# Optimization experiments

Hardware: AMD Instinct MI355X
Metric: run time of the kernel (lower is better)

## Reference

```python
import jax, jax.numpy as jnp
import numpy as np

D_MODEL = 256
HIDDEN = 64
R = 1            # corr_radius
MAX_DELTA = 4.0  # max_delta_px
GROUPS = 8       # _gn_groups(64)
B, H, W = 2, 128, 128


def grid_sample_border(img, grid):
    """Bilinear grid_sample, padding_mode='border', align_corners=False.
    img: [B,C,H,W], grid: [B,Hg,Wg,2] (x,y in [-1,1]-ish). -> [B,C,Hg,Wg]"""
    Bi, C, Hi, Wi = img.shape
    x = (grid[..., 0] + 1.0) * (Wi * 0.5) - 0.5
    y = (grid[..., 1] + 1.0) * (Hi * 0.5) - 0.5
    x = jnp.clip(x, 0.0, Wi - 1.0)
    y = jnp.clip(y, 0.0, Hi - 1.0)
    x0 = jnp.floor(x); y0 = jnp.floor(y)
    wx = (x - x0)[:, None]; wy = (y - y0)[:, None]
    x0i = x0.astype(jnp.int32); y0i = y0.astype(jnp.int32)
    x1i = jnp.minimum(x0i + 1, Wi - 1); y1i = jnp.minimum(y0i + 1, Hi - 1)
    imgf = img.reshape(Bi, C, Hi * Wi)
    def gat(im, yi, xi):  # im [C,HW], yi/xi [Hg,Wg]
        return im[:, (yi * Wi + xi).reshape(-1)].reshape(C, *yi.shape)
    g = jax.vmap(gat)
    v00 = g(imgf, y0i, x0i); v01 = g(imgf, y0i, x1i)
    v10 = g(imgf, y1i, x0i); v11 = g(imgf, y1i, x1i)
    return (v00 * (1 - wx) * (1 - wy) + v01 * wx * (1 - wy)
            + v10 * (1 - wx) * wy + v11 * wx * wy)


def l2norm(x, axis):
    n = jnp.sqrt(jnp.sum(x * x, axis=axis, keepdims=True))
    return x / jnp.maximum(n, 1e-12)


def conv2d(x, w, pad):
    return jax.lax.conv_general_dilated(x, w, (1, 1), [(pad, pad), (pad, pad)],
                                        dimension_numbers=('NCHW', 'OIHW', 'NCHW'))


def group_norm(x, gamma, beta, groups=GROUPS, eps=1e-5):
    Bi, C, Hi, Wi = x.shape
    xg = x.reshape(Bi, groups, C // groups, Hi, Wi)
    mu = xg.mean(axis=(2, 3, 4), keepdims=True)
    var = xg.var(axis=(2, 3, 4), keepdims=True)
    xn = ((xg - mu) * jax.lax.rsqrt(var + eps)).reshape(Bi, C, Hi, Wi)
    return xn * gamma[None, :, None, None] + beta[None, :, None, None]


def conv_gn_gelu(x, w, g, b, pad):
    return jax.nn.gelu(group_norm(conv2d(x, w, pad), g, b), approximate=False)


def make_grid(h, w):
    xs = (jnp.arange(w, dtype=jnp.float32) + 0.5) * (2.0 / w) - 1.0
    ys = (jnp.arange(h, dtype=jnp.float32) + 0.5) * (2.0 / h) - 1.0
    gx, gy = jnp.meshgrid(xs, ys, indexing='xy')
    return jnp.stack([gx, gy], axis=-1)[None]  # [1,H,W,2]


def setup_inputs() -> dict:
    key = jax.random.key(0)
    ks = jax.random.split(key, 12)
    in_ch = D_MODEL * 3 + 2 + 1 + (2 * R + 1) ** 2  # 780
    def w(k, o, i, kh, kw):
        return (jax.random.normal(k, (o, i, kh, kw), jnp.float32)
                / np.sqrt(i * kh * kw).astype(np.float32))
    return {
        'feat_A_map': jax.random.normal(ks[0], (B, D_MODEL, H, W), jnp.float32),
        'feat_B_map': jax.random.normal(ks[1], (B, D_MODEL, H, W), jnp.float32),
        'coarse_warp': jax.random.uniform(ks[2], (B, H, W, 2), jnp.float32, -1.0, 1.0),
        'confidence': jax.random.uniform(ks[3], (B, H, W), jnp.float32),
        'enc1_w': w(ks[4], HIDDEN, in_ch, 1, 1),
        'gn1_g': jnp.ones(HIDDEN, jnp.float32), 'gn1_b': jnp.zeros(HIDDEN, jnp.float32),
        'enc2_w': w(ks[5], HIDDEN, HIDDEN, 3, 3),
        'gn2_g': jnp.ones(HIDDEN, jnp.float32), 'gn2_b': jnp.zeros(HIDDEN, jnp.float32),
        'enc3_w': w(ks[6], HIDDEN, HIDDEN, 3, 3),
        'gn3_g': jnp.ones(HIDDEN, jnp.float32), 'gn3_b': jnp.zeros(HIDDEN, jnp.float32),
        'delta_w': w(ks[7], 2, HIDDEN, 3, 3) * 0.01, 'delta_b': jnp.zeros(2, jnp.float32),
        'conf_w': w(ks[8], 1, HIDDEN, 3, 3) * 0.01, 'conf_b': jnp.zeros(1, jnp.float32),
    }


def reference(feat_A_map, feat_B_map, coarse_warp, confidence,
              enc1_w, gn1_g, gn1_b, enc2_w, gn2_g, gn2_b, enc3_w, gn3_g, gn3_b,
              delta_w, delta_b, conf_w, conf_b):
    cw = jnp.clip(jnp.nan_to_num(coarse_warp, nan=0.0, posinf=1.5, neginf=-1.5), -1.5, 1.5)
    route = jax.lax.stop_gradient(cw)  # detached routing warp
    warped_B = grid_sample_border(feat_B_map, route)
    src = make_grid(H, W)
    disp = jnp.transpose(cw - src, (0, 3, 1, 2))  # [B,2,H,W]
    conf = jnp.clip(jnp.nan_to_num(confidence, nan=0.0, posinf=1.0, neginf=0.0), 0.0, 1.0)
    conf_chw = conf[:, None]
    # warp-aware correlation over (2R+1)^2 offsets, vectorized via vmap
    fa_n = l2norm(jnp.nan_to_num(feat_A_map, nan=0.0, posinf=0.0, neginf=0.0), axis=1)
    fb = jnp.nan_to_num(feat_B_map, nan=0.0, posinf=0.0, neginf=0.0)
    offs = jnp.asarray([[2.0 * dx / W, 2.0 * dy / H]
                        for dy in range(-R, R + 1) for dx in range(-R, R + 1)],
                       dtype=jnp.float32)  # [K,2]
    grids = jnp.clip(jnp.nan_to_num(route[None] + offs[:, None, None, None, :],
                                    nan=0.0, posinf=1.5, neginf=-1.5), -1.5, 1.5)
    sampled = jax.vmap(grid_sample_border, in_axes=(None, 0))(fb, grids)  # [K,B,C,H,W]
    corr = jnp.transpose(jnp.sum(fa_n[None] * l2norm(sampled, axis=2), axis=2),
                         (1, 0, 2, 3))  # [B,K,H,W]
    x = jnp.concatenate([feat_A_map, warped_B, jnp.abs(feat_A_map - warped_B),
                         disp, conf_chw, corr], axis=1)
    h = conv_gn_gelu(x, enc1_w, gn1_g, gn1_b, 0)
    h = conv_gn_gelu(h, enc2_w, gn2_g, gn2_b, 1)
    h = conv_gn_gelu(h, enc3_w, gn3_g, gn3_b, 1)
    delta_raw = jnp.transpose(jnp.tanh(conv2d(h, delta_w, 1)
                                       + delta_b[None, :, None, None]), (0, 2, 3, 1))
    scale = jnp.asarray([2.0 * MAX_DELTA / W, 2.0 * MAX_DELTA / H], jnp.float32)
    fine_warp = jnp.clip(jnp.nan_to_num(route + delta_raw * scale,
                                        nan=0.0, posinf=1.5, neginf=-1.5), -1.5, 1.5)
    conf_delta = (conv2d(h, conf_w, 1) + conf_b[None, :, None, None])[:, 0]
    p = jnp.clip(conf, 1e-4, 1.0 - 1e-4)
    base_logit = jnp.log(p) - jnp.log1p(-p)
    refined_logits = base_logit + 0.5 * conf_delta
    refined_conf = jnp.clip(jax.nn.sigmoid(refined_logits), 0.0, 1.0)
    return (fine_warp, refined_conf, refined_logits)
```

## Files before the change

### kernel.cpp

```cpp
#include <hip/hip_runtime.h>
#include <hip/hip_bf16.h>
#include <math.h>

#define B_ 2
#define H_ 128
#define W_ 128
#define C_ 256
#define HID 64
#define PIX_PER (H_*W_)
#define NPIX (B_*PIX_PER)
#define K1STEPS 25
#define K3STEPS 18
#define SROW 264

using f32x4 = __attribute__((ext_vector_type(4))) float;
using s16x8 = __attribute__((ext_vector_type(8))) short;
using u16x2 = __attribute__((ext_vector_type(2))) unsigned short;
using u16x4 = __attribute__((ext_vector_type(4))) unsigned short;
using u16x8 = __attribute__((ext_vector_type(8))) unsigned short;

__device__ __forceinline__ float bf2f(unsigned short u) {
    return __uint_as_float(((unsigned)u) << 16);
}
__device__ __forceinline__ unsigned short f2bf(float f) {
    unsigned u = __float_as_uint(f);
    u += 0x7FFFu + ((u >> 16) & 1u);
    return (unsigned short)(u >> 16);
}
__device__ __forceinline__ float clean15(float v) {
    if (v != v) v = 0.f;
    return fminf(fmaxf(v, -1.5f), 1.5f);
}
__device__ __forceinline__ float clean01(float v) {
    if (v != v) v = 0.f;
    return fminf(fmaxf(v, 0.f), 1.f);
}

__global__ __launch_bounds__(256) void k_transpose(const float* __restrict__ A,
                                                   const float* __restrict__ Bm,
                                                   unsigned short* __restrict__ faT,
                                                   unsigned short* __restrict__ fbT,
                                                   const float* __restrict__ w1,
                                                   const float* __restrict__ w2,
                                                   const float* __restrict__ w3,
                                                   unsigned short* __restrict__ p1,
                                                   unsigned short* __restrict__ p2,
                                                   unsigned short* __restrict__ p3)
{
    if (blockIdx.z == 4) {
        if (blockIdx.y != 0 || blockIdx.x >= 61) return;
        int t = blockIdx.x * 256 + threadIdx.x;
        if (t < 6400) {
            int lane = t & 63, nt = (t >> 6) & 3, ks = t >> 8;
            int n = nt * 16 + (lane & 15);
            int kb = ks * 32 + 8 * (lane >> 4);
#pragma unroll
            for (int j = 0; j < 8; j++) {
                int k = kb + j;
                p1[(size_t)t * 8 + j] = (k < 780) ? f2bf(w1[(size_t)n * 780 + k]) : (unsigned short)0;
            }
        } else if (t < 6400 + 2 * 4608) {
            int which = (t - 6400) / 4608;
            int idx = (t - 6400) % 4608;
            const float* w = which ? w3 : w2;
            unsigned short* p = which ? p3 : p2;
            int lane = idx & 63, nt = (idx >> 6) & 3, ks = idx >> 8;
            int n = nt * 16 + (lane & 15);
            int tap = ks >> 1;
            int ky = tap / 3, kx = tap % 3;
#pragma unroll
            for (int j = 0; j < 8; j++) {
                int c = (ks & 1) * 32 + 8 * (lane >> 4) + j;
                p[(size_t)idx * 8 + j] = f2bf(w[(((size_t)n * 64 + c) * 3 + ky) * 3 + kx]);
            }
        }
        return;
    }
    __shared__ float tile[32][33];
    int hw0 = blockIdx.x * 32;
    int c0  = blockIdx.y * 32;
    int z   = blockIdx.z;
    int b   = z >> 1;
    const float* src = (z & 1) ? Bm : A;
    unsigned short* dst = (z & 1) ? fbT : faT;
    int tx = threadIdx.x & 31, ty = threadIdx.x >> 5;
    const float* s = src + ((size_t)b * C_ + c0) * (size_t)PIX_PER + hw0;
#pragma unroll
    for (int i = 0; i < 32; i += 8) {
        float v = s[(size_t)(ty + i) * PIX_PER + tx];
        if (!isfinite(v)) v = 0.f;
        tile[ty + i][tx] = v;
    }
    __syncthreads();
    unsigned short* d = dst + ((size_t)b * PIX_PER + hw0) * C_ + c0;
    int pr = threadIdx.x & 7;
    int hw = threadIdx.x >> 3;
    u16x4 o;
#pragma unroll
    for (int j = 0; j < 4; j++) o[j] = f2bf(tile[4 * pr + j][hw]);
    *(u16x4*)(d + (size_t)hw * C_ + 4 * pr) = o;
}

__global__ __launch_bounds__(256) void k_sample(const float* __restrict__ cw,
                                                const float* __restrict__ confp,
                                                const unsigned short* __restrict__ faT,
                                                const unsigned short* __restrict__ fbT,
                                                unsigned short* __restrict__ wbbuf,
                                                unsigned short* __restrict__ tail)
{
    __shared__ unsigned short S[4][17 * SROW];
    __shared__ float CT[4][16 * 20 + 4];
    int lane = threadIdx.x & 63;
    int wv = threadIdx.x >> 6;
    int wid = blockIdx.x * 4 + wv;
    int b = wid >> 14, y = (wid >> 7) & 127, x = wid & 127;

    float gx = clean15(cw[(size_t)wid * 2 + 0]);
    float gy = clean15(cw[(size_t)wid * 2 + 1]);
    float conf = clean01(confp[wid]);

    float pxu = (gx + 1.f) * 64.f - 0.5f;
    float pyu = (gy + 1.f) * 64.f - 0.5f;
    float x0f = floorf(pxu), y0f = floorf(pyu);
    float wx = pxu - x0f, wy = pyu - y0f;
    int x0 = (int)x0f, y0 = (int)y0f;
    int co[4], ro[4];
#pragma unroll
    for (int k = 0; k < 4; k++) {
        co[k] = min(max(x0 - 1 + k, 0), 127) << 8;
        ro[k] = min(max(y0 - 1 + k, 0), 127) << 15;
    }
    const unsigned short* fbP = fbT + ((size_t)b << 22);

    int h = lane >> 5, lo = lane & 31;
    u16x8 stg[8];
#pragma unroll
    for (int i = 0; i < 8; i++) {
        int rr = ro[i >> 1];
        int cc = h ? co[((i & 1) << 1) + 1] : co[(i & 1) << 1];
        stg[i] = *(const u16x8*)(fbP + rr + cc + lo * 8);
    }
    u16x8 stfa;
    if (h == 0) stfa = *(const u16x8*)(faT + (size_t)wid * C_ + lo * 8);

    unsigned short* Sw = &S[wv][0];
#pragma unroll
    for (int i = 0; i < 8; i++)
        *(u16x8*)(Sw + (2 * i + h) * SROW + lo * 8) = stg[i];
    if (h == 0) *(u16x8*)(Sw + 16 * SROW + lo * 8) = stfa;

    int q = lane & 15;
    int tA = (q == 0) ? 16 : q - 1;
    int koff = (lane >> 4) * 8;
    const unsigned short* pA = Sw + tA * SROW + koff;
    const unsigned short* pB = Sw + q * SROW + koff;
    f32x4 acc = {0.f, 0.f, 0.f, 0.f};
#pragma unroll
    for (int ks = 0; ks < 8; ks++) {
        s16x8 av = *(const s16x8*)(pA + ks * 32);
        s16x8 bv = *(const s16x8*)(pB + ks * 32);
        acc = __builtin_amdgcn_mfma_f32_16x16x32_bf16(av, bv, acc, 0, 0, 0);
    }
    *(f32x4*)&CT[wv][q * 20 + (lane >> 4) * 4] = acc;

    float w00 = (1.f - wx) * (1.f - wy), w01 = wx * (1.f - wy);
    float w10 = (1.f - wx) * wy,         w11 = wx * wy;
    u16x4 v5  = *(const u16x4*)(Sw + 5 * SROW + lane * 4);
    u16x4 v6  = *(const u16x4*)(Sw + 6 * SROW + lane * 4);
    u16x4 v9  = *(const u16x4*)(Sw + 9 * SROW + lane * 4);
    u16x4 v10 = *(const u16x4*)(Sw + 10 * SROW + lane * 4);
    u16x4 v15 = *(const u16x4*)(Sw + 15 * SROW + lane * 4);
    u16x4 vfa = *(const u16x4*)(Sw + 16 * SROW + lane * 4);
    float fa2p = 0.f, t152p = 0.f;
    u16x4 wbo;
#pragma unroll
    for (int i = 0; i < 4; i++) {
        float s = w00 * bf2f(v5[i]) + w01 * bf2f(v6[i])
                + w10 * bf2f(v9[i]) + w11 * bf2f(v10[i]);
        wbo[i] = f2bf(s);
        float fv = bf2f(vfa[i]), tv = bf2f(v15[i]);
        fa2p  += fv * fv;
        t152p += tv * tv;
    }
    *(u16x4*)(wbbuf + (size_t)wid * C_ + lane * 4) = wbo;
#pragma unroll
    for (int m = 1; m < 64; m <<= 1) {
        fa2p  += __shfl_xor(fa2p, m);
        t152p += __shfl_xor(t152p, m);
    }

    if (lane < 32) {
        float outv = 0.f;
        if (lane == 0)      outv = gx - (((float)x + 0.5f) * 0.015625f - 1.f);
        else if (lane == 1) outv = gy - (((float)y + 0.5f) * 0.015625f - 1.f);
        else if (lane == 2) outv = conf;
        else if (lane < 12) {
            int j = lane - 3;
            int jd = j / 3, jm = j - jd * 3;
            int m00 = jd * 4 + jm;
            const float* Cw = &CT[wv][0];
            float D00 = Cw[m00 * 20], D01 = Cw[(m00 + 1) * 20];
            float D10 = Cw[(m00 + 4) * 20], D11 = Cw[(m00 + 5) * 20];
            float dot = w00 * D00 + w01 * D01 + w10 * D10 + w11 * D11;
#define GR(a, b) Cw[(b) * 20 + (a) + 1]
            float g11 = (j == 8) ? t152p : GR(m00 + 5, m00 + 5);
            float s2 = w00 * w00 * GR(m00, m00) + w01 * w01 * GR(m00 + 1, m00 + 1)
                     + w10 * w10 * GR(m00 + 4, m00 + 4) + w11 * w11 * g11
                     + 2.f * (w00 * w01 * GR(m00, m00 + 1) + w00 * w10 * GR(m00, m00 + 4)
                            + w00 * w11 * GR(m00, m00 + 5) + w01 * w10 * GR(m00 + 1, m00 + 4)
                            + w01 * w11 * GR(m00 + 1, m00 + 5) + w10 * w11 * GR(m00 + 4, m00 + 5));
#undef GR
            outv = dot * rsqrtf(fmaxf(fa2p, 1e-24f)) * rsqrtf(fmaxf(s2, 1e-24f));
        }
        tail[(size_t)wid * 32 + lane] = f2bf(outv);
    }
}

__device__ __forceinline__ void gn_epilogue(const f32x4 acc[4], float* lds,
                                            float* __restrict__ pbuf, int bid,
                                            int la, int lb, int wv)
{
    int d = la >> 3;
    int slot = wv * 32 + lb * 8 + (la & 7);
#pragma unroll
    for (int nt = 0; nt < 4; nt++) {
        float s  = acc[nt][0] + acc[nt][1] + acc[nt][2] + acc[nt][3];
        float s2 = acc[nt][0] * acc[nt][0] + acc[nt][1] * acc[nt][1]
                 + acc[nt][2] * acc[nt][2] + acc[nt][3] * acc[nt][3];
        int g = nt * 2 + d;
        lds[(g * 128 + slot) * 2 + 0] = s;
        lds[(g * 128 + slot) * 2 + 1] = s2;
    }
    __syncthreads();
    int tid = threadIdx.x;
    int g = tid >> 5, i = tid & 31;
    float s  = lds[(g * 128 + i) * 2]     + lds[(g * 128 + i + 32) * 2]
             + lds[(g * 128 + i + 64) * 2] + lds[(g * 128 + i + 96) * 2];
    float s2 = lds[(g * 128 + i) * 2 + 1]     + lds[(g * 128 + i + 32) * 2 + 1]
             + lds[(g * 128 + i + 64) * 2 + 1] + lds[(g * 128 + i + 96) * 2 + 1];
#pragma unroll
    for (int m = 1; m < 32; m <<= 1) { s += __shfl_xor(s, m); s2 += __shfl_xor(s2, m); }
    if (i == 0) {
        pbuf[(bid * 8 + g) * 2]     = s;
        pbuf[(bid * 8 + g) * 2 + 1] = s2;
    }
}

__global__ __launch_bounds__(256) void k_gemm1(const unsigned short* __restrict__ faT,
                                               const unsigned short* __restrict__ wbbuf,
                                               const unsigned short* __restrict__ tail,
                                               const unsigned short* __restrict__ pack,
                                               unsigned short* __restrict__ hpre,
                                               float* __restrict__ pbuf)
{
    __shared__ float lds[8 * 128 * 2];
    int wave = (blockIdx.x * 256 + threadIdx.x) >> 6;
    int lane = threadIdx.x & 63;
    int la = lane & 15, lb = lane >> 4;
    int row = wave * 16 + la;
    const unsigned short* fa_row = faT   + (size_t)row * C_ + lb * 8;
    const unsigned short* wb_row = wbbuf + (size_t)row * C_ + lb * 8;
    f32x4 acc[4] = {{0,0,0,0},{0,0,0,0},{0,0,0,0},{0,0,0,0}};

#pragma unroll
    for (int ks = 0; ks < 8; ks++) {
        s16x8 a = *(const s16x8*)(fa_row + ks * 32);
#pragma unroll
        for (int nt = 0; nt < 4; nt++)
            acc[nt] = __builtin_amdgcn_mfma_f32_16x16x32_bf16(a,
                *(const s16x8*)(pack + ((size_t)(ks * 4 + nt) * 64 + lane) * 8), acc[nt], 0, 0, 0);
    }
#pragma unroll
    for (int ks = 0; ks < 8; ks++) {
        s16x8 a = *(const s16x8*)(wb_row + ks * 32);
#pragma unroll
        for (int nt = 0; nt < 4; nt++)
            acc[nt] = __builtin_amdgcn_mfma_f32_16x16x32_bf16(a,
                *(const s16x8*)(pack + ((size_t)((ks + 8) * 4 + nt) * 64 + lane) * 8), acc[nt], 0, 0, 0);
    }
#pragma unroll
    for (int ks = 0; ks < 8; ks++) {
        u16x8 av = *(const u16x8*)(fa_row + ks * 32);
        u16x8 bv = *(const u16x8*)(wb_row + ks * 32);
        s16x8 a;
#pragma unroll
        for (int j = 0; j < 8; j++)
            a[j] = (short)f2bf(fabsf(bf2f(av[j]) - bf2f(bv[j])));
#pragma unroll
        for (int nt = 0; nt < 4; nt++)
            acc[nt] = __builtin_amdgcn_mfma_f32_16x16x32_bf16(a,
                *(const s16x8*)(pack + ((size_t)((ks + 16) * 4 + nt) * 64 + lane) * 8), acc[nt], 0, 0, 0);
    }
    {
        s16x8 a = *(const s16x8*)(tail + (size_t)row * 32 + lb * 8);
#pragma unroll
        for (int nt = 0; nt < 4; nt++)
            acc[nt] = __builtin_amdgcn_mfma_f32_16x16x32_bf16(a,
                *(const s16x8*)(pack + ((size_t)(24 * 4 + nt) * 64 + lane) * 8), acc[nt], 0, 0, 0);
    }

    int orow = wave * 16 + lb * 4;
#pragma unroll
    for (int nt = 0; nt < 4; nt++)
#pragma unroll
        for (int r = 0; r < 4; r++)
            hpre[(size_t)(orow + r) * HID + nt * 16 + la] = f2bf(acc[nt][r]);

    gn_epilogue(acc, lds, pbuf, blockIdx.x, la, lb, (threadIdx.x >> 6));
}

__global__ __launch_bounds__(256) void k_convgn(const unsigned short* __restrict__ hin,
                                                const float* __restrict__ gamma,
                                                const float* __restrict__ beta,
                                                const float* __restrict__ pbin,
                                                const unsigned short* __restrict__ pack,
                                                unsigned short* __restrict__ hout,
                                                float* __restrict__ pbout)
{
    __shared__ unsigned short T[8 * 100 * 8];
    __shared__ float eplds[8 * 128 * 2];
    __shared__ float sm[16];
    int tid = threadIdx.x;
    int bid = blockIdx.x;
    int b = bid >> 8;
    int tile = bid & 255;
    int ty0 = (tile >> 4) << 3, tx0 = (tile & 15) << 3;

    {
        int g = tid >> 5, i = tid & 31;
        float s = 0.f, s2 = 0.f;
#pragma unroll
        for (int k = 0; k < 8; k++) {
            int pb = b * 256 + i + k * 32;
            s  += pbin[(pb * 8 + g) * 2];
            s2 += pbin[(pb * 8 + g) * 2 + 1];
        }
#pragma unroll
        for (int m = 1; m < 32; m <<= 1) { s += __shfl_xor(s, m); s2 += __shfl_xor(s2, m); }
        if (i == 0) {
            const float inv = 1.f / 131072.f;
            float mean = s * inv;
            float var = fmaxf(s2 * inv - mean * mean, 0.f);
            sm[g * 2] = mean;
            sm[g * 2 + 1] = rsqrtf(var + 1e-5f);
        }
    }
    __syncthreads();

#pragma unroll
    for (int pass = 0; pass < 4; pass++) {
        int idx = pass * 256 + tid;
        if (idx < 800) {
            int c8 = idx & 7, slot = idx >> 3;
            int py = slot / 10, px = slot - py * 10;
            int gy = ty0 + py - 1, gx = tx0 + px - 1;
            u16x8 o = {0, 0, 0, 0, 0, 0, 0, 0};
            if ((unsigned)gy < 128u && (unsigned)gx < 128u) {
                int gpix = (b << 14) + (gy << 7) + gx;
                u16x8 v = *(const u16x8*)(hin + (size_t)gpix * HID + c8 * 8);
                float mean = sm[c8 * 2], rstd = sm[c8 * 2 + 1];
#pragma unroll
                for (int i = 0; i < 8; i++) {
                    int c = c8 * 8 + i;
                    float xn = (bf2f(v[i]) - mean) * rstd * gamma[c] + beta[c];
                    o[i] = f2bf(0.5f * xn * (1.f + erff(xn * 0.70710678118654752f)));
                }
            }
            *(u16x8*)(&T[(c8 * 100 + slot) * 8]) = o;
        }
    }
    __syncthreads();

    int lane = tid & 63, wv = tid >> 6;
    int la = lane & 15, lb = lane >> 4;
    int ay = la >> 3, ax = la & 7;
    f32x4 acc[4] = {{0,0,0,0},{0,0,0,0},{0,0,0,0},{0,0,0,0}};
#pragma unroll
    for (int ks = 0; ks < K3STEPS; ks++) {
        int tap = ks >> 1;
        int dy = tap / 3, dx = tap - dy * 3;
        int c8 = (ks & 1) * 4 + lb;
        int py = wv * 2 + ay + dy;
        int px = ax + dx;
        s16x8 a = *(const s16x8*)(&T[(c8 * 100 + py * 10 + px) * 8]);
#pragma unroll
        for (int nt = 0; nt < 4; nt++)
            acc[nt] = __builtin_amdgcn_mfma_f32_16x16x32_bf16(a,
                *(const s16x8*)(pack + ((size_t)(ks * 4 + nt) * 64 + lane) * 8), acc[nt], 0, 0, 0);
    }

#pragma unroll
    for (int nt = 0; nt < 4; nt++)
#pragma unroll
        for (int r = 0; r < 4; r++) {
            int po = lb * 4 + r;
            int yy = ty0 + wv * 2 + (po >> 3);
            int xx = tx0 + (po & 7);
            hout[((size_t)((b << 14) + (yy << 7) + xx)) * HID + nt * 16 + la] = f2bf(acc[nt][r]);
        }

    gn_epilogue(acc, eplds, pbout, bid, la, lb, wv);
}

__global__ __launch_bounds__(256) void k_gnfinal(const unsigned short* __restrict__ hpre,
                                                 const float* __restrict__ gamma,
                                                 const float* __restrict__ beta,
                                                 const float* __restrict__ pbuf,
                                                 const float* __restrict__ cw,
                                                 const float* __restrict__ confp,
                                                 const float* __restrict__ dw,
                                                 const float* __restrict__ db,
                                                 const float* __restrict__ cwgt,
                                                 const float* __restrict__ cb,
                                                 float* __restrict__ out)
{
    __shared__ unsigned short hnT[100 * 68];
    __shared__ float wds[1154];
    __shared__ float wcs[577];
    __shared__ float sm[16];
    int tid = threadIdx.x;
    int bid = blockIdx.x;
    int b = bid >> 8;
    int tile = bid & 255;
    int ty0 = (tile >> 4) << 3, tx0 = (tile & 15) << 3;

    for (int i = tid; i < 1152; i += 256) wds[i] = dw[i];
    for (int i = tid; i < 576; i += 256) wcs[i] = cwgt[i];
    if (tid == 0) { wds[1152] = db[0]; wds[1153] = db[1]; wcs[576] = cb[0]; }

    {
        int g = tid >> 5, i = tid & 31;
        float s = 0.f, s2 = 0.f;
#pragma unroll
        for (int k = 0; k < 8; k++) {
            int pb = b * 256 + i + k * 32;
            s  += pbuf[(pb * 8 + g) * 2];
            s2 += pbuf[(pb * 8 + g) * 2 + 1];
        }
#pragma unroll
        for (int m = 1; m < 32; m <<= 1) { s += __shfl_xor(s, m); s2 += __shfl_xor(s2, m); }
        if (i == 0) {
            const float inv = 1.f / 131072.f;
            float mean = s * inv;
            float var = fmaxf(s2 * inv - mean * mean, 0.f);
            sm[g * 2] = mean;
            sm[g * 2 + 1] = rsqrtf(var + 1e-5f);
        }
    }
    __syncthreads();

#pragma unroll
    for (int pass = 0; pass < 4; pass++) {
        int idx = pass * 256 + tid;
        if (idx < 800) {
            int slot = idx >> 3, c8 = idx & 7;
            int py = slot / 10, px = slot - py * 10;
            int gy = ty0 + py - 1, gx = tx0 + px - 1;
            u16x8 o = {0, 0, 0, 0, 0, 0, 0, 0};
            if ((unsigned)gy < 128u && (unsigned)gx < 128u) {
                int gpix = (b << 14) + (gy << 7) + gx;
                u16x8 v = *(const u16x8*)(hpre + (size_t)gpix * HID + c8 * 8);
                float mean = sm[c8 * 2], rstd = sm[c8 * 2 + 1];
#pragma unroll
                for (int i = 0; i < 8; i++) {
                    int c = c8 * 8 + i;
                    float xn = (bf2f(v[i]) - mean) * rstd * gamma[c] + beta[c];
                    float ge = 0.5f * xn * (1.f + erff(xn * 0.70710678118654752f));
                    o[i] = f2bf(ge);
                }
            }
            *(u16x8*)(&hnT[slot * 68 + c8 * 8]) = o;
        }
    }
    __syncthreads();

    int p = tid >> 2, part = tid & 3;
    int py = (p >> 3) + 1, px = (p & 7) + 1;
    float d0 = 0.f, d1 = 0.f, c0 = 0.f;
#pragma unroll
    for (int ky = 0; ky < 3; ky++)
#pragma unroll
        for (int kx = 0; kx < 3; kx++) {
            const unsigned short* hp = &hnT[((py + ky - 1) * 10 + (px + kx - 1)) * 68];
            int widx = ky * 3 + kx;
#pragma unroll
            for (int cc = 0; cc < 2; cc++) {
                int c8 = part * 2 + cc;
                u16x8 v = *(const u16x8*)(hp + c8 * 8);
#pragma unroll
                for (int i = 0; i < 8; i++) {
                    float f = bf2f(v[i]);
                    int c = c8 * 8 + i;
                    d0 += f * wds[c * 9 + widx];
                    d1 += f * wds[576 + c * 9 + widx];
                    c0 += f * wcs[c * 9 + widx];
                }
            }
        }
#pragma unroll
    for (int m = 1; m < 4; m <<= 1) {
        d0 += __shfl_xor(d0, m);
        d1 += __shfl_xor(d1, m);
        c0 += __shfl_xor(c0, m);
    }
    if (part == 0) {
        int pix = (b << 14) + ((ty0 + py - 1) << 7) + (tx0 + px - 1);
        d0 = tanhf(d0 + wds[1152]);
        d1 = tanhf(d1 + wds[1153]);
        c0 += wcs[576];

        float gx = clean15(cw[(size_t)pix * 2 + 0]);
        float gy = clean15(cw[(size_t)pix * 2 + 1]);
        float fwx = fminf(fmaxf(gx + d0 * 0.0625f, -1.5f), 1.5f);
        float fwy = fminf(fmaxf(gy + d1 * 0.0625f, -1.5f), 1.5f);

        float conf = clean01(confp[pix]);
        float pp = fminf(fmaxf(conf, 1e-4f), 1.f - 1e-4f);
        float bl = logf(pp) - log1pf(-pp);
        float rl = bl + 0.5f * c0;
        float rc = fminf(fmaxf(1.f / (1.f + expf(-rl)), 0.f), 1.f);

        out[(size_t)pix * 2 + 0] = fwx;
        out[(size_t)pix * 2 + 1] = fwy;
        out[(size_t)NPIX * 2 + pix] = rc;
        out[(size_t)NPIX * 2 + NPIX + pix] = rl;
    }
}

extern "C" void kernel_launch(void* const* d_in, const int* in_sizes, int n_in,
                              void* d_out, int out_size, void* d_ws, size_t ws_size,
                              hipStream_t stream)
{
    const float* feat_A = (const float*)d_in[0];
    const float* feat_B = (const float*)d_in[1];
    const float* cw     = (const float*)d_in[2];
    const float* conf   = (const float*)d_in[3];
    const float* w1     = (const float*)d_in[4];
    const float* g1     = (const float*)d_in[5];
    const float* b1     = (const float*)d_in[6];
    const float* w2     = (const float*)d_in[7];
    const float* g2     = (const float*)d_in[8];
    const float* b2     = (const float*)d_in[9];
    const float* w3     = (const float*)d_in[10];
    const float* g3     = (const float*)d_in[11];
    const float* b3     = (const float*)d_in[12];
    const float* dw     = (const float*)d_in[13];
    const float* db     = (const float*)d_in[14];
    const float* cwgt   = (const float*)d_in[15];
    const float* cb     = (const float*)d_in[16];
    float* out = (float*)d_out;

    char* w = (char*)d_ws;
    size_t o = 0;
    unsigned short* faT  = (unsigned short*)(w + o); o += (size_t)NPIX * C_ * 2;
    unsigned short* fbT  = (unsigned short*)(w + o); o += (size_t)NPIX * C_ * 2;
    unsigned short* wbb  = (unsigned short*)(w + o); o += (size_t)NPIX * C_ * 2;
    unsigned short* tail = (unsigned short*)(w + o); o += (size_t)NPIX * 32 * 2;
    unsigned short* hA   = (unsigned short*)(w + o); o += (size_t)NPIX * HID * 2;
    unsigned short* hB   = (unsigned short*)(w + o); o += (size_t)NPIX * HID * 2;
    unsigned short* p1   = (unsigned short*)(w + o); o += (size_t)K1STEPS * 4 * 64 * 8 * 2;
    unsigned short* p2   = (unsigned short*)(w + o); o += (size_t)K3STEPS * 4 * 64 * 8 * 2;
    unsigned short* p3   = (unsigned short*)(w + o); o += (size_t)K3STEPS * 4 * 64 * 8 * 2;
    float* pbuf1 = (float*)(w + o); o += 512 * 8 * 2 * 4;
    float* pbuf2 = (float*)(w + o); o += 512 * 8 * 2 * 4;
    float* pbuf3 = (float*)(w + o); o += 512 * 8 * 2 * 4;

    k_transpose<<<dim3(PIX_PER / 32, C_ / 32, 5), 256, 0, stream>>>(feat_A, feat_B, faT, fbT,
                                                                    w1, w2, w3, p1, p2, p3);
    k_sample<<<NPIX / 4, 256, 0, stream>>>(cw, conf, faT, fbT, wbb, tail);

    k_gemm1<<<(NPIX / 16) / 4, 256, 0, stream>>>(faT, wbb, tail, p1, hA, pbuf1);
    k_convgn<<<512, 256, 0, stream>>>(hA, g1, b1, pbuf1, p2, hB, pbuf2);
    k_convgn<<<512, 256, 0, stream>>>(hB, g2, b2, pbuf2, p3, hA, pbuf3);
    k_gnfinal<<<512, 256, 0, stream>>>(hA, g3, b3, pbuf3, cw, conf,
                                       dw, db, cwgt, cb, out);
}
```

Before: 126.0 us.

## Split 3x3 conv tiles into 8x4 blocks and divide output channels across waves

The 3x3 conv+GN kernels now run 1024 blocks over 8x4 pixel tiles instead of 512 blocks over 8x8. Each pair of waves shares a pixel row pair and splits the 64 output channels, so each wave holds two accumulators instead of four. This is meant to raise occupancy and parallelism, at the cost of a larger halo overhead per tile (60 slots for 32 pixels). The group-norm partial sums are now reduced in-kernel with shuffles into a small LDS array, which doubles the partial-buffer size consumers must read. The SROW padding constant also changes.

```diff
diff --git a/kernel.cpp b/kernel.cpp
--- a/kernel.cpp
+++ b/kernel.cpp
@@ -11,7 +11,7 @@
 #define NPIX (B_*PIX_PER)
 #define K1STEPS 25
 #define K3STEPS 18
-#define SROW 264
+#define SROW 258
 
 using f32x4 = __attribute__((ext_vector_type(4))) float;
 using s16x8 = __attribute__((ext_vector_type(8))) short;
@@ -313,25 +313,25 @@
                                                 const float* __restrict__ gamma,
                                                 const float* __restrict__ beta,
                                                 const float* __restrict__ pbin,
+                                                int npbb,
                                                 const unsigned short* __restrict__ pack,
                                                 unsigned short* __restrict__ hout,
                                                 float* __restrict__ pbout)
 {
-    __shared__ unsigned short T[8 * 100 * 8];
-    __shared__ float eplds[8 * 128 * 2];
+    __shared__ unsigned short T[8 * 60 * 8];
+    __shared__ float ep[4][4][2];
     __shared__ float sm[16];
     int tid = threadIdx.x;
     int bid = blockIdx.x;
-    int b = bid >> 8;
-    int tile = bid & 255;
-    int ty0 = (tile >> 4) << 3, tx0 = (tile & 15) << 3;
+    int b = bid >> 9;
+    int tile = bid & 511;
+    int ty0 = (tile >> 4) << 2, tx0 = (tile & 15) << 3;
 
     {
         int g = tid >> 5, i = tid & 31;
         float s = 0.f, s2 = 0.f;
-#pragma unroll
-        for (int k = 0; k < 8; k++) {
-            int pb = b * 256 + i + k * 32;
+        for (int k = 0; k < (npbb >> 5); k++) {
+            int pb = b * npbb + i + k * 32;
             s  += pbin[(pb * 8 + g) * 2];
             s2 += pbin[(pb * 8 + g) * 2 + 1];
         }
@@ -348,9 +348,9 @@
     __syncthreads();
 
 #pragma unroll
-    for (int pass = 0; pass < 4; pass++) {
+    for (int pass = 0; pass < 2; pass++) {
         int idx = pass * 256 + tid;
-        if (idx < 800) {
+        if (idx < 480) {
             int c8 = idx & 7, slot = idx >> 3;
             int py = slot / 10, px = slot - py * 10;
             int gy = ty0 + py - 1, gx = tx0 + px - 1;
@@ -366,40 +366,67 @@
                     o[i] = f2bf(0.5f * xn * (1.f + erff(xn * 0.70710678118654752f)));
                 }
             }
-            *(u16x8*)(&T[(c8 * 100 + slot) * 8]) = o;
+            *(u16x8*)(&T[(c8 * 60 + slot) * 8]) = o;
         }
     }
     __syncthreads();
 
     int lane = tid & 63, wv = tid >> 6;
+    int rp = wv >> 1, hh = wv & 1;
     int la = lane & 15, lb = lane >> 4;
     int ay = la >> 3, ax = la & 7;
-    f32x4 acc[4] = {{0,0,0,0},{0,0,0,0},{0,0,0,0},{0,0,0,0}};
+    f32x4 acc[2] = {{0,0,0,0},{0,0,0,0}};
 #pragma unroll
     for (int ks = 0; ks < K3STEPS; ks++) {
         int tap = ks >> 1;
         int dy = tap / 3, dx = tap - dy * 3;
         int c8 = (ks & 1) * 4 + lb;
-        int py = wv * 2 + ay + dy;
+        int py = rp * 2 + ay + dy;
         int px = ax + dx;
-        s16x8 a = *(const s16x8*)(&T[(c8 * 100 + py * 10 + px) * 8]);
-#pragma unroll
-        for (int nt = 0; nt < 4; nt++)
-            acc[nt] = __builtin_amdgcn_mfma_f32_16x16x32_bf16(a,
-                *(const s16x8*)(pack + ((size_t)(ks * 4 + nt) * 64 + lane) * 8), acc[nt], 0, 0, 0);
-    }
-
-#pragma unroll
-    for (int nt = 0; nt < 4; nt++)
+        s16x8 a = *(const s16x8*)(&T[(c8 * 60 + py * 10 + px) * 8]);
+#pragma unroll
+        for (int j = 0; j < 2; j++) {
+            int nt = 2 * hh + j;
+            acc[j] = __builtin_amdgcn_mfma_f32_16x16x32_bf16(a,
+                *(const s16x8*)(pack + ((size_t)(ks * 4 + nt) * 64 + lane) * 8), acc[j], 0, 0, 0);
+        }
+    }
+
+#pragma unroll
+    for (int j = 0; j < 2; j++) {
+        int nt = 2 * hh + j;
 #pragma unroll
         for (int r = 0; r < 4; r++) {
             int po = lb * 4 + r;
-            int yy = ty0 + wv * 2 + (po >> 3);
+            int yy = ty0 + rp * 2 + (po >> 3);
             int xx = tx0 + (po & 7);
-            hout[((size_t)((b << 14) + (yy << 7) + xx)) * HID + nt * 16 + la] = f2bf(acc[nt][r]);
-        }
-
-    gn_epilogue(acc, eplds, pbout, bid, la, lb, wv);
+            hout[((size_t)((b << 14) + (yy << 7) + xx)) * HID + nt * 16 + la] = f2bf(acc[j][r]);
+        }
+    }
+
+#pragma unroll
+    for (int j = 0; j < 2; j++) {
+        float s  = acc[j][0] + acc[j][1] + acc[j][2] + acc[j][3];
+        float s2 = acc[j][0]*acc[j][0] + acc[j][1]*acc[j][1]
+                 + acc[j][2]*acc[j][2] + acc[j][3]*acc[j][3];
+#pragma unroll
+        for (int m = 1; m < 64; m <<= 1) {
+            if (m == 8) continue;
+            s  += __shfl_xor(s, m);
+            s2 += __shfl_xor(s2, m);
+        }
+        if (lane == 0 || lane == 8) {
+            ep[wv][j * 2 + (lane >> 3)][0] = s;
+            ep[wv][j * 2 + (lane >> 3)][1] = s2;
+        }
+    }
+    __syncthreads();
+    if (tid < 8) {
+        int g = tid;
+        int hx = g >> 2, gl = g & 3;
+        pbout[(bid * 8 + g) * 2]     = ep[hx][gl][0] + ep[hx + 2][gl][0];
+        pbout[(bid * 8 + g) * 2 + 1] = ep[hx][gl][1] + ep[hx + 2][gl][1];
+    }
 }
 
 __global__ __launch_bounds__(256) void k_gnfinal(const unsigned short* __restrict__ hpre,
@@ -432,8 +459,8 @@
         int g = tid >> 5, i = tid & 31;
         float s = 0.f, s2 = 0.f;
 #pragma unroll
-        for (int k = 0; k < 8; k++) {
-            int pb = b * 256 + i + k * 32;
+        for (int k = 0; k < 16; k++) {
+            int pb = b * 512 + i + k * 32;
             s  += pbuf[(pb * 8 + g) * 2];
             s2 += pbuf[(pb * 8 + g) * 2 + 1];
         }
@@ -561,17 +588,17 @@
     unsigned short* p1   = (unsigned short*)(w + o); o += (size_t)K1STEPS * 4 * 64 * 8 * 2;
     unsigned short* p2   = (unsigned short*)(w + o); o += (size_t)K3STEPS * 4 * 64 * 8 * 2;
     unsigned short* p3   = (unsigned short*)(w + o); o += (size_t)K3STEPS * 4 * 64 * 8 * 2;
-    float* pbuf1 = (float*)(w + o); o += 512 * 8 * 2 * 4;
-    float* pbuf2 = (float*)(w + o); o += 512 * 8 * 2 * 4;
-    float* pbuf3 = (float*)(w + o); o += 512 * 8 * 2 * 4;
+    float* pbuf1 = (float*)(w + o); o += 1024 * 8 * 2 * 4;
+    float* pbuf2 = (float*)(w + o); o += 1024 * 8 * 2 * 4;
+    float* pbuf3 = (float*)(w + o); o += 1024 * 8 * 2 * 4;
 
     k_transpose<<<dim3(PIX_PER / 32, C_ / 32, 5), 256, 0, stream>>>(feat_A, feat_B, faT, fbT,
                                                                     w1, w2, w3, p1, p2, p3);
     k_sample<<<NPIX / 4, 256, 0, stream>>>(cw, conf, faT, fbT, wbb, tail);
 
     k_gemm1<<<(NPIX / 16) / 4, 256, 0, stream>>>(faT, wbb, tail, p1, hA, pbuf1);
-    k_convgn<<<512, 256, 0, stream>>>(hA, g1, b1, pbuf1, p2, hB, pbuf2);
-    k_convgn<<<512, 256, 0, stream>>>(hB, g2, b2, pbuf2, p3, hA, pbuf3);
+    k_convgn<<<1024, 256, 0, stream>>>(hA, g1, b1, pbuf1, 256, p2, hB, pbuf2);
+    k_convgn<<<1024, 256, 0, stream>>>(hB, g2, b2, pbuf2, 512, p3, hA, pbuf3);
     k_gnfinal<<<512, 256, 0, stream>>>(hA, g3, b3, pbuf3, cw, conf,
                                        dw, db, cwgt, cb, out);
 }
```

Result: slower. 192.9 us (+53.1%).
